# Kernel optimization log

Measured on AMD Instinct MI355X. Metric: run time of the kernel, lower is better.

## Reference

```python
import jax, jax.numpy as jnp
import numpy as np

DIM = 256
H = 4
HD = DIM // H
SCALE = HD ** -0.5
W = 10
PAD = W // 2
MAX_LEN = 512


def setup_inputs() -> dict:
    key = jax.random.key(0)
    ks = jax.random.split(key, 32)
    B, T, D = 32, 512, DIM
    def w(k, shape):
        return jax.random.normal(k, shape, dtype=jnp.float32) * 0.02
    inp = {
        'x': jax.random.normal(ks[0], (B, T, D), dtype=jnp.float32),
        # global TemporalAttention params (weights stored as (in,out))
        'gq_w': w(ks[1], (D, D)), 'gq_b': jnp.zeros((D,), jnp.float32),
        'gk_w': w(ks[2], (D, D)), 'gk_b': jnp.zeros((D,), jnp.float32),
        'gv_w': w(ks[3], (D, D)), 'gv_b': jnp.zeros((D,), jnp.float32),
        'go_w': w(ks[4], (D, D)), 'go_b': jnp.zeros((D,), jnp.float32),
        'rel_pos_bias': w(ks[5], (2 * MAX_LEN - 1, H)),
        # local sliding-window attention params
        'lq_w': w(ks[6], (D, D)), 'lq_b': jnp.zeros((D,), jnp.float32),
        'lk_w': w(ks[7], (D, D)), 'lk_b': jnp.zeros((D,), jnp.float32),
        'lv_w': w(ks[8], (D, D)), 'lv_b': jnp.zeros((D,), jnp.float32),
        # pattern attention (only q/k projections matter for returned weights)
        'pattern_embed': jax.random.normal(ks[9], (1, 3, D), dtype=jnp.float32),
        'pq_w': w(ks[10], (D, D)), 'pq_b': jnp.zeros((D,), jnp.float32),
        'pk_w': w(ks[11], (D, D)), 'pk_b': jnp.zeros((D,), jnp.float32),
        # fusion MLP
        'f1_w': w(ks[12], (2 * D, D)), 'f1_b': jnp.zeros((D,), jnp.float32),
        'f2_w': w(ks[13], (D, D)), 'f2_b': jnp.zeros((D,), jnp.float32),
    }
    return inp


def _forward(x, gq_w, gq_b, gk_w, gk_b, gv_w, gv_b, go_w, go_b, rel_pos_bias,
             lq_w, lq_b, lk_w, lk_b, lv_w, lv_b,
             pattern_embed, pq_w, pq_b, pk_w, pk_b,
             f1_w, f1_b, f2_w, f2_b):
    B, T, D = x.shape
    # ---- global temporal attention ----
    q = (x @ gq_w + gq_b).reshape(B, T, H, HD)
    k = (x @ gk_w + gk_b).reshape(B, T, H, HD)
    v = (x @ gv_w + gv_b).reshape(B, T, H, HD)
    attn = jnp.einsum('bthd,bshd->bhts', q, k) * SCALE  # (B,H,T,T)
    pos = jnp.arange(T)
    idx = jnp.clip(pos[None, :] - pos[:, None] + T - 1, 0, 2 * T - 2)  # (T,T)
    attn = attn + jnp.transpose(rel_pos_bias[idx], (2, 0, 1))[None]
    attn_w = jax.nn.softmax(attn, axis=-1)  # dropout = identity in eval
    g_out = jnp.einsum('bhts,bshd->bthd', attn_w, v).reshape(B, T, D)
    global_out = g_out @ go_w + go_b
    # ---- local sliding-window attention (single head over full dim) ----
    x_pad = jnp.pad(x, ((0, 0), (PAD, PAD), (0, 0)))  # zero pad -> k/v get bias
    lq = x @ lq_w + lq_b                      # (B,T,D)
    lk = x_pad @ lk_w + lk_b                  # (B,T+W,D)
    lv = x_pad @ lv_w + lv_b
    widx = jnp.arange(T)[:, None] + jnp.arange(W)[None, :]  # (T,W)
    k_win = lk[:, widx]                       # (B,T,W,D)
    v_win = lv[:, widx]
    l_attn = jax.nn.softmax(jnp.einsum('btd,btwd->btw', lq, k_win) * SCALE, axis=-1)
    local_out = jnp.einsum('btw,btwd->btd', l_attn, v_win)
    # ---- fusion MLP + residual ----
    fused = jnp.concatenate([global_out, local_out], axis=-1)
    output = jax.nn.relu(fused @ f1_w + f1_b) @ f2_w + f2_b + x
    # ---- pattern attention (torch MHA, weights averaged over heads) ----
    pe = jnp.broadcast_to(pattern_embed, (B, 3, D))
    pooled = jnp.mean(x, axis=1, keepdims=True)  # (B,1,D)
    pq = (pooled @ pq_w + pq_b).reshape(B, 1, H, HD)
    pk = (pe @ pk_w + pk_b).reshape(B, 3, H, HD)
    plogits = jnp.einsum('bqhd,bkhd->bhqk', pq, pk) * SCALE  # (B,H,1,3)
    pw = jax.nn.softmax(plogits, axis=-1).mean(axis=1)  # avg over heads -> (B,1,3)
    pattern_scores = pw[:, 0]  # (B,3)
    return output, pattern_scores


def reference(x, gq_w, gq_b, gk_w, gk_b, gv_w, gv_b, go_w, go_b, rel_pos_bias,
              lq_w, lq_b, lk_w, lk_b, lv_w, lv_b,
              pattern_embed, pq_w, pq_b, pk_w, pk_b,
              f1_w, f1_b, f2_w, f2_b):
    return _forward(x, gq_w, gq_b, gk_w, gk_b, gv_w, gv_b, go_w, go_b, rel_pos_bias,
                    lq_w, lq_b, lk_w, lk_b, lv_w, lv_b,
                    pattern_embed, pq_w, pq_b, pk_w, pk_b,
                    f1_w, f1_b, f2_w, f2_b)
```

## Files before the change

### kernel.cpp

```cpp
#include <hip/hip_runtime.h>
#include <hip/hip_bf16.h>

typedef __attribute__((ext_vector_type(8))) __bf16 bf16x8;
typedef __attribute__((ext_vector_type(8))) unsigned short u16x8;
typedef __attribute__((ext_vector_type(4))) float f32x4;

#define MFMA_BF16(a,b,c) __builtin_amdgcn_mfma_f32_16x16x32_bf16((a),(b),(c),0,0,0)

#define ASCALE 0.125f
#define SEQT 512
#define NB 32
#define BT 16384

#define GLD_LDS16(g, l) __builtin_amdgcn_global_load_lds( \
    (__attribute__((address_space(1))) void*)(g), \
    (__attribute__((address_space(3))) void*)(l), 16, 0, 0)

__device__ __forceinline__ unsigned short f2bf(float f) {
    unsigned int u = __float_as_uint(f);
    u += 0x7fffu + ((u >> 16) & 1u);
    return (unsigned short)(u >> 16);
}
__device__ __forceinline__ float bf2f(unsigned short h) {
    return __uint_as_float(((unsigned int)h) << 16);
}

__global__ __launch_bounds__(256) void cast_x_kernel(const float* __restrict__ x,
                                                     unsigned short* __restrict__ xb, int n) {
    int i = (blockIdx.x * 256 + threadIdx.x) * 4;
    if (i < n) {
        float4 v = *(const float4*)(x + i);
        ushort4 o;
        o.x = f2bf(v.x); o.y = f2bf(v.y); o.z = f2bf(v.z); o.w = f2bf(v.w);
        *(ushort4*)(xb + i) = o;
    }
}

struct WPack {
    const float* src[9];
    unsigned short* dst[9];
    int K[9];
    const float* bsrc[5];
    float* bdst;
};

__global__ __launch_bounds__(256) void wconv_all(WPack p) {
    const int z = blockIdx.z;
    const int tid = threadIdx.x;
    if (z == 9) {
        int idx = blockIdx.y * 8 + blockIdx.x;
        if (idx < 5) p.bdst[idx * 256 + tid] = p.bsrc[idx][tid];
        return;
    }
    const int K = p.K[z];
    const int k0 = blockIdx.x * 64;
    if (k0 >= K) return;
    const int n0 = blockIdx.y * 64;
    __shared__ float tile[64][65];
    const int tx = tid & 63, ty = tid >> 6;
    const float* src = p.src[z];
    #pragma unroll
    for (int i = 0; i < 16; ++i) {
        int r = ty * 16 + i;
        tile[r][tx] = src[(size_t)(k0 + r) * 256 + n0 + tx];
    }
    __syncthreads();
    unsigned short* dst = p.dst[z];
    #pragma unroll
    for (int i = 0; i < 16; ++i) {
        int r = ty * 16 + i;
        dst[(size_t)(n0 + r) * K + k0 + tx] = f2bf(tile[tx][r]);
    }
}

template<int BM, int BN>
__global__ __launch_bounds__(256)
void gemm_v3(const unsigned short* __restrict__ A, const unsigned short* __restrict__ Bt,
             const float* __restrict__ bias, int K,
             void* __restrict__ out, int ldc, int mode, int do_relu, int bias_row,
             const float* __restrict__ resid) {
    constexpr int CA = BM / 32;
    constexpr int CB = BN / 32;
    constexpr int MFM = 4;
    constexpr int MFN = (BM == 128) ? 4 : 2;
    __shared__ __align__(16) unsigned short As[2][BM * 64];
    __shared__ __align__(16) unsigned short Bs[2][BN * 64];
    const int tid = threadIdx.x;
    const int w = tid >> 6, l = tid & 63, g = l >> 4, rl = l & 15;
    const int wrow = (BM == 128) ? (w >> 1) * 64 : 0;
    const int wcol = (BM == 128) ? (w & 1) * 64 : w * 32;
    const int m0 = blockIdx.x * BM, n0 = blockIdx.y * BN;

    f32x4 acc[MFM][MFN];
    #pragma unroll
    for (int m = 0; m < MFM; ++m)
        #pragma unroll
        for (int n = 0; n < MFN; ++n) acc[m][n] = (f32x4){0.f, 0.f, 0.f, 0.f};

    auto stage = [&](int buf, int k0) {
        #pragma unroll
        for (int j = 0; j < CA; ++j) {
            int e = j * 256 + tid;
            int r = e >> 3, sp = e & 7;
            int kc = (sp ^ (r & 7)) * 8;
            GLD_LDS16(A + (size_t)(m0 + r) * K + k0 + kc, &As[buf][e * 8]);
        }
        #pragma unroll
        for (int j = 0; j < CB; ++j) {
            int e = j * 256 + tid;
            int r = e >> 3, sp = e & 7;
            int kc = (sp ^ (r & 7)) * 8;
            GLD_LDS16(Bt + (size_t)(n0 + r) * K + k0 + kc, &Bs[buf][e * 8]);
        }
    };

    const int NIT = K >> 6;
    stage(0, 0);
    const int sx = (rl & 7);
    for (int it = 0; it < NIT; ++it) {
        const int cur = it & 1;
        if (it + 1 < NIT) {
            stage(cur ^ 1, (it + 1) << 6);
            asm volatile("s_waitcnt vmcnt(%0)" :: "n"(CA + CB) : "memory");
        } else {
            asm volatile("s_waitcnt vmcnt(0)" ::: "memory");
        }
        __builtin_amdgcn_s_barrier();
        #pragma unroll
        for (int kk = 0; kk < 2; ++kk) {
            const int co = ((kk * 4 + g) ^ sx) * 8;
            bf16x8 af[MFM], bf_[MFN];
            #pragma unroll
            for (int m = 0; m < MFM; ++m)
                af[m] = *(const bf16x8*)&As[cur][(wrow + m * 16 + rl) * 64 + co];
            #pragma unroll
            for (int n = 0; n < MFN; ++n)
                bf_[n] = *(const bf16x8*)&Bs[cur][(wcol + n * 16 + rl) * 64 + co];
            #pragma unroll
            for (int m = 0; m < MFM; ++m)
                #pragma unroll
                for (int n = 0; n < MFN; ++n)
                    acc[m][n] = MFMA_BF16(af[m], bf_[n], acc[m][n]);
        }
        __builtin_amdgcn_s_barrier();
    }

    #pragma unroll
    for (int m = 0; m < MFM; ++m) {
        #pragma unroll
        for (int n = 0; n < MFN; ++n) {
            #pragma unroll
            for (int r = 0; r < 4; ++r) {
                int row = m0 + wrow + m * 16 + g * 4 + r;
                int col = n0 + wcol + n * 16 + rl;
                float v = acc[m][n][r] + (bias_row ? bias[row] : bias[col]);
                if (do_relu) v = fmaxf(v, 0.f);
                if (mode == 0) {
                    ((unsigned short*)out)[(size_t)row * ldc + col] = f2bf(v);
                } else {
                    float res = resid ? resid[(size_t)row * ldc + col] : 0.f;
                    ((float*)out)[(size_t)row * ldc + col] = v + res;
                }
            }
        }
    }
}

__global__ __launch_bounds__(256)
void attn_global2(const unsigned short* __restrict__ proj, const unsigned short* __restrict__ vT,
                  const float* __restrict__ rpb, unsigned short* __restrict__ gout) {
    __shared__ __align__(16) unsigned short Ks[64][72];
    __shared__ __align__(16) unsigned short Vs[64][72];
    __shared__ __align__(16) unsigned short Ps[64][72];
    __shared__ float rb_s[127];

    const int tid = threadIdx.x;
    const int w = tid >> 6, l = tid & 63, g = l >> 4, rl = l & 15;
    const int bh = blockIdx.y, b = bh >> 2, h = bh & 3;
    const int t0 = blockIdx.x * 64;

    bf16x8 qf[2];
    #pragma unroll
    for (int kk = 0; kk < 2; ++kk)
        qf[kk] = *(const bf16x8*)(proj + (size_t)(b * SEQT + t0 + w * 16 + rl) * 1280
                                  + h * 64 + kk * 32 + g * 8);

    f32x4 oacc[4];
    #pragma unroll
    for (int n = 0; n < 4; ++n) oacc[n] = (f32x4){0.f, 0.f, 0.f, 0.f};
    float lpart[4] = {0.f, 0.f, 0.f, 0.f};

    for (int s0 = 0; s0 < SEQT; s0 += 64) {
        __syncthreads();
        #pragma unroll
        for (int cc = 0; cc < 2; ++cc) {
            int c = tid + cc * 256;
            int sr = c >> 3, hc = c & 7;
            u16x8 kv = *(const u16x8*)(proj + (size_t)(b * SEQT + s0 + sr) * 1280
                                       + 256 + h * 64 + hc * 8);
            *(u16x8*)&Ks[sr][hc * 8] = kv;
            u16x8 vv = *(const u16x8*)(vT + (size_t)(h * 64 + sr) * BT
                                       + b * SEQT + s0 + hc * 8);
            *(u16x8*)&Vs[sr][hc * 8] = vv;
        }
        if (tid < 127) {
            int dd = s0 - t0 + 448 + tid;
            rb_s[tid] = rpb[dd * 4 + h];
        }
        __syncthreads();

        f32x4 sacc[4];
        #pragma unroll
        for (int n = 0; n < 4; ++n) sacc[n] = (f32x4){0.f, 0.f, 0.f, 0.f};
        #pragma unroll
        for (int kk = 0; kk < 2; ++kk) {
            #pragma unroll
            for (int n = 0; n < 4; ++n) {
                bf16x8 kf = *(const bf16x8*)&Ks[n * 16 + rl][kk * 32 + g * 8];
                sacc[n] = MFMA_BF16(qf[kk], kf, sacc[n]);
            }
        }

        #pragma unroll
        for (int n = 0; n < 4; ++n) {
            #pragma unroll
            for (int r = 0; r < 4; ++r) {
                int relc = (n * 16 + rl) - (w * 16 + g * 4 + r) + 63;
                float p = __expf(sacc[n][r] * ASCALE + rb_s[relc]);
                lpart[r] += p;
                Ps[w * 16 + g * 4 + r][n * 16 + rl] = f2bf(p);
            }
        }

        #pragma unroll
        for (int kk = 0; kk < 2; ++kk) {
            bf16x8 pf = *(const bf16x8*)&Ps[w * 16 + rl][kk * 32 + g * 8];
            #pragma unroll
            for (int n = 0; n < 4; ++n) {
                bf16x8 vf = *(const bf16x8*)&Vs[n * 16 + rl][kk * 32 + g * 8];
                oacc[n] = MFMA_BF16(pf, vf, oacc[n]);
            }
        }
    }

    #pragma unroll
    for (int r = 0; r < 4; ++r) {
        #pragma unroll
        for (int mk = 1; mk < 16; mk <<= 1) lpart[r] += __shfl_xor(lpart[r], mk);
    }
    const size_t obase = (size_t)b * SEQT * 256 + h * 64;
    #pragma unroll
    for (int n = 0; n < 4; ++n) {
        #pragma unroll
        for (int r = 0; r < 4; ++r) {
            float o = oacc[n][r] / lpart[r];
            gout[obase + (size_t)(t0 + w * 16 + g * 4 + r) * 256 + n * 16 + rl] = f2bf(o);
        }
    }
}

__global__ __launch_bounds__(256)
void local_attn(const unsigned short* __restrict__ proj,
                const float* __restrict__ lk_bias, const float* __restrict__ lv_bias,
                unsigned short* __restrict__ fused) {
    const int tid = threadIdx.x;
    const int wv = tid >> 6, lane = tid & 63;
    const int row = blockIdx.x * 4 + wv;
    const int b = row >> 9, tt = row & 511;

    ushort4 qv = *((const ushort4*)(proj + (size_t)row * 1280 + 512) + lane);
    float qf[4] = {bf2f(qv.x), bf2f(qv.y), bf2f(qv.z), bf2f(qv.w)};

    float sw[10];
    #pragma unroll
    for (int w = 0; w < 10; ++w) {
        int src = tt + w - 5;
        float kf[4];
        if (src >= 0 && src < 512) {
            ushort4 kv = *((const ushort4*)(proj + (size_t)(b * 512 + src) * 1280 + 768) + lane);
            kf[0] = bf2f(kv.x); kf[1] = bf2f(kv.y); kf[2] = bf2f(kv.z); kf[3] = bf2f(kv.w);
        } else {
            float4 kb4 = *((const float4*)lk_bias + lane);
            kf[0] = kb4.x; kf[1] = kb4.y; kf[2] = kb4.z; kf[3] = kb4.w;
        }
        float p = qf[0] * kf[0] + qf[1] * kf[1] + qf[2] * kf[2] + qf[3] * kf[3];
        #pragma unroll
        for (int mk = 1; mk < 64; mk <<= 1) p += __shfl_xor(p, mk);
        sw[w] = p * ASCALE;
    }
    float mx = sw[0];
    #pragma unroll
    for (int w = 1; w < 10; ++w) mx = fmaxf(mx, sw[w]);
    float pv[10], s = 0.f;
    #pragma unroll
    for (int w = 0; w < 10; ++w) { pv[w] = __expf(sw[w] - mx); s += pv[w]; }
    float inv = 1.f / s;

    float of[4] = {0.f, 0.f, 0.f, 0.f};
    #pragma unroll
    for (int w = 0; w < 10; ++w) {
        int src = tt + w - 5;
        float vf[4];
        if (src >= 0 && src < 512) {
            ushort4 vv = *((const ushort4*)(proj + (size_t)(b * 512 + src) * 1280 + 1024) + lane);
            vf[0] = bf2f(vv.x); vf[1] = bf2f(vv.y); vf[2] = bf2f(vv.z); vf[3] = bf2f(vv.w);
        } else {
            float4 vb4 = *((const float4*)lv_bias + lane);
            vf[0] = vb4.x; vf[1] = vb4.y; vf[2] = vb4.z; vf[3] = vb4.w;
        }
        float pw = pv[w] * inv;
        of[0] += pw * vf[0]; of[1] += pw * vf[1]; of[2] += pw * vf[2]; of[3] += pw * vf[3];
    }
    ushort4 o;
    o.x = f2bf(of[0]); o.y = f2bf(of[1]); o.z = f2bf(of[2]); o.w = f2bf(of[3]);
    *((ushort4*)(fused + (size_t)row * 512 + 256) + lane) = o;
}

__global__ __launch_bounds__(256)
void pooled_part(const unsigned short* __restrict__ xb, float* __restrict__ pp) {
    int b = blockIdx.x >> 3, tc = blockIdx.x & 7;
    int d = threadIdx.x;
    const unsigned short* xp = xb + ((size_t)b * SEQT + tc * 64) * 256 + d;
    float s = 0.f;
    #pragma unroll 8
    for (int t = 0; t < 64; ++t) s += bf2f(xp[(size_t)t * 256]);
    pp[(size_t)(tc * 32 + b) * 256 + d] = s * (1.0f / 512.0f);
}

__global__ __launch_bounds__(256)
void pattern_k(const float* __restrict__ pp, const float* __restrict__ pe,
               const float* __restrict__ pq_w, const float* __restrict__ pq_b,
               const float* __restrict__ pk_w, const float* __restrict__ pk_b,
               float* __restrict__ out_scores) {
    __shared__ float pool_s[256];
    __shared__ float pes[3 * 256];
    __shared__ float pq_s[256];
    __shared__ float pk_s[3][256];
    __shared__ float pw_s[4][3];
    int b = blockIdx.x, d = threadIdx.x;
    float ps = 0.f;
    #pragma unroll
    for (int tc = 0; tc < 8; ++tc) ps += pp[(size_t)(tc * 32 + b) * 256 + d];
    pool_s[d] = ps;
    pes[d] = pe[d]; pes[256 + d] = pe[256 + d]; pes[512 + d] = pe[512 + d];
    __syncthreads();
    float acc = pq_b[d];
    for (int k = 0; k < 256; ++k) acc += pool_s[k] * pq_w[k * 256 + d];
    pq_s[d] = acc;
    for (int j = 0; j < 3; ++j) {
        float a = pk_b[d];
        for (int k = 0; k < 256; ++k) a += pes[j * 256 + k] * pk_w[k * 256 + d];
        pk_s[j][d] = a;
    }
    __syncthreads();
    int h = d >> 6, lane = d & 63;
    float lg[3];
    #pragma unroll
    for (int j = 0; j < 3; ++j) {
        float p = pq_s[h * 64 + lane] * pk_s[j][h * 64 + lane];
        #pragma unroll
        for (int mk = 1; mk < 64; mk <<= 1) p += __shfl_xor(p, mk);
        lg[j] = p * ASCALE;
    }
    float mx = fmaxf(fmaxf(lg[0], lg[1]), lg[2]);
    float e0 = __expf(lg[0] - mx), e1 = __expf(lg[1] - mx), e2 = __expf(lg[2] - mx);
    float sinv = 1.f / (e0 + e1 + e2);
    if (lane == 0) { pw_s[h][0] = e0 * sinv; pw_s[h][1] = e1 * sinv; pw_s[h][2] = e2 * sinv; }
    __syncthreads();
    if (d < 3)
        out_scores[b * 3 + d] = 0.25f * (pw_s[0][d] + pw_s[1][d] + pw_s[2][d] + pw_s[3][d]);
}

extern "C" void kernel_launch(void* const* d_in, const int* in_sizes, int n_in,
                              void* d_out, int out_size, void* d_ws, size_t ws_size,
                              hipStream_t stream) {
    (void)in_sizes; (void)n_in; (void)out_size; (void)ws_size;
    const float* x    = (const float*)d_in[0];
    const float* gq_w = (const float*)d_in[1];  const float* gq_b = (const float*)d_in[2];
    const float* gk_w = (const float*)d_in[3];  const float* gk_b = (const float*)d_in[4];
    const float* gv_w = (const float*)d_in[5];  const float* gv_b = (const float*)d_in[6];
    const float* go_w = (const float*)d_in[7];  const float* go_b = (const float*)d_in[8];
    const float* rpb  = (const float*)d_in[9];
    const float* lq_w = (const float*)d_in[10]; const float* lq_b = (const float*)d_in[11];
    const float* lk_w = (const float*)d_in[12]; const float* lk_b = (const float*)d_in[13];
    const float* lv_w = (const float*)d_in[14]; const float* lv_b = (const float*)d_in[15];
    const float* pe   = (const float*)d_in[16];
    const float* pq_w = (const float*)d_in[17]; const float* pq_b = (const float*)d_in[18];
    const float* pk_w = (const float*)d_in[19]; const float* pk_b = (const float*)d_in[20];
    const float* f1_w = (const float*)d_in[21]; const float* f1_b = (const float*)d_in[22];
    const float* f2_w = (const float*)d_in[23]; const float* f2_b = (const float*)d_in[24];

    char* ws = (char*)d_ws;
    const size_t MB = 1024 * 1024;
    unsigned short* xb    = (unsigned short*)(ws + 0);
    unsigned short* proj  = (unsigned short*)(ws + 8 * MB);
    unsigned short* vT    = (unsigned short*)(ws + 48 * MB);
    unsigned short* fused = (unsigned short*)(ws + 56 * MB);
    unsigned short* hb    = (unsigned short*)(ws + 72 * MB);
    unsigned short* wts   = (unsigned short*)(ws + 80 * MB);
    unsigned short* gv_t  = wts;
    unsigned short* go_t  = gv_t + 65536;
    unsigned short* f1_t  = go_t + 65536;
    unsigned short* f2_t  = f1_t + 131072;
    unsigned short* wcat  = f2_t + 65536;
    float* bcat = (float*)(ws + 82 * MB);
    float* pp   = (float*)(ws + 83 * MB);

    float* out = (float*)d_out;
    float* out_scores = out + (size_t)BT * 256;

    cast_x_kernel<<<4096, 256, 0, stream>>>(x, xb, BT * 256);
    WPack p;
    p.src[0] = gq_w; p.dst[0] = wcat + 0 * 65536; p.K[0] = 256;
    p.src[1] = gk_w; p.dst[1] = wcat + 1 * 65536; p.K[1] = 256;
    p.src[2] = lq_w; p.dst[2] = wcat + 2 * 65536; p.K[2] = 256;
    p.src[3] = lk_w; p.dst[3] = wcat + 3 * 65536; p.K[3] = 256;
    p.src[4] = lv_w; p.dst[4] = wcat + 4 * 65536; p.K[4] = 256;
    p.src[5] = gv_w; p.dst[5] = gv_t;  p.K[5] = 256;
    p.src[6] = go_w; p.dst[6] = go_t;  p.K[6] = 256;
    p.src[7] = f1_w; p.dst[7] = f1_t;  p.K[7] = 512;
    p.src[8] = f2_w; p.dst[8] = f2_t;  p.K[8] = 256;
    p.bsrc[0] = gq_b; p.bsrc[1] = gk_b; p.bsrc[2] = lq_b; p.bsrc[3] = lk_b; p.bsrc[4] = lv_b;
    p.bdst = bcat;
    wconv_all<<<dim3(8, 4, 10), 256, 0, stream>>>(p);
    pooled_part<<<256, 256, 0, stream>>>(xb, pp);

    gemm_v3<128, 128><<<dim3(BT / 128, 10), 256, 0, stream>>>(xb, wcat, bcat, 256, proj, 1280, 0, 0, 0, nullptr);
    gemm_v3<64, 128><<<dim3(4, BT / 128), 256, 0, stream>>>(gv_t, xb, gv_b, 256, vT, BT, 0, 0, 1, nullptr);

    attn_global2<<<dim3(SEQT / 64, NB * 4), 256, 0, stream>>>(proj, vT, rpb, xb);

    gemm_v3<64, 128><<<dim3(BT / 64, 2), 256, 0, stream>>>(xb, go_t, go_b, 256, fused, 512, 0, 0, 0, nullptr);

    local_attn<<<BT / 4, 256, 0, stream>>>(proj, lk_b, lv_b, fused);

    gemm_v3<64, 128><<<dim3(BT / 64, 2), 256, 0, stream>>>(fused, f1_t, f1_b, 512, hb, 256, 0, 1, 0, nullptr);
    gemm_v3<64, 128><<<dim3(BT / 64, 2), 256, 0, stream>>>(hb, f2_t, f2_b, 256, out, 256, 1, 0, 0, x);

    pattern_k<<<NB, 256, 0, stream>>>(pp, pe, pq_w, pq_b, pk_w, pk_b, out_scores);
}
```

Baseline: 306.2 us.

## Fold output projection into first fusion MLP weight and retile GEMM to K=32

Precomputes go_w·f1_w[:256] as a combined weight (and the matching folded bias) so the global-attention output projection GEMM is removed. Attention now writes straight into the fused buffer, and the first MLP GEMM uses the combined weight. The GEMM kernel is also rewritten with a K-step of 32 and a 2x2 wave layout with configurable leading dimensions. The folded weight is rounded to bf16, which adds a little rounding error. The smaller K tile doubles the loop iterations and barriers.

```diff
diff --git a/kernel.cpp b/kernel.cpp
--- a/kernel.cpp
+++ b/kernel.cpp
@@ -42,6 +42,7 @@
     int K[9];
     const float* bsrc[5];
     float* bdst;
+    unsigned short* w1cat;
 };
 
 __global__ __launch_bounds__(256) void wconv_all(WPack p) {
@@ -56,39 +57,59 @@
     const int k0 = blockIdx.x * 64;
     if (k0 >= K) return;
     const int n0 = blockIdx.y * 64;
-    __shared__ float tile[64][65];
     const int tx = tid & 63, ty = tid >> 6;
     const float* src = p.src[z];
+    unsigned short* dst = p.dst[z];
+    if (z == 6) {
+        #pragma unroll
+        for (int i = 0; i < 16; ++i) {
+            int r = ty * 16 + i;
+            dst[(size_t)(k0 + r) * 256 + n0 + tx] = f2bf(src[(size_t)(k0 + r) * 256 + n0 + tx]);
+        }
+        return;
+    }
+    __shared__ float tile[64][65];
     #pragma unroll
     for (int i = 0; i < 16; ++i) {
         int r = ty * 16 + i;
         tile[r][tx] = src[(size_t)(k0 + r) * 256 + n0 + tx];
     }
     __syncthreads();
-    unsigned short* dst = p.dst[z];
     #pragma unroll
     for (int i = 0; i < 16; ++i) {
         int r = ty * 16 + i;
-        dst[(size_t)(n0 + r) * K + k0 + tx] = f2bf(tile[tx][r]);
-    }
-}
-
-template<int BM, int BN>
-__global__ __launch_bounds__(256)
-void gemm_v3(const unsigned short* __restrict__ A, const unsigned short* __restrict__ Bt,
+        unsigned short v = f2bf(tile[tx][r]);
+        dst[(size_t)(n0 + r) * K + k0 + tx] = v;
+        if (z == 7 && k0 >= 256)
+            p.w1cat[(size_t)(n0 + r) * 512 + k0 + tx] = v;
+    }
+}
+
+__global__ __launch_bounds__(256)
+void bias2_k(const float* __restrict__ f1_b, const float* __restrict__ go_b,
+             const float* __restrict__ f1_w, float* __restrict__ f1bp) {
+    int n = threadIdx.x;
+    float s = f1_b[n];
+    for (int k = 0; k < 256; ++k) s += go_b[k] * f1_w[k * 256 + n];
+    f1bp[n] = s;
+}
+
+template<int BM>
+__global__ __launch_bounds__(256)
+void gemm_v5(const unsigned short* __restrict__ A, int lda,
+             const unsigned short* __restrict__ Bt, int ldb,
              const float* __restrict__ bias, int K,
              void* __restrict__ out, int ldc, int mode, int do_relu, int bias_row,
              const float* __restrict__ resid) {
-    constexpr int CA = BM / 32;
-    constexpr int CB = BN / 32;
-    constexpr int MFM = 4;
-    constexpr int MFN = (BM == 128) ? 4 : 2;
-    __shared__ __align__(16) unsigned short As[2][BM * 64];
-    __shared__ __align__(16) unsigned short Bs[2][BN * 64];
+    constexpr int BN = 128;
+    constexpr int AR = BM / 64, BR = BN / 64;
+    constexpr int MFM = BM / 32, MFN = 4;
+    __shared__ __align__(16) unsigned short As[2][BM * 32];
+    __shared__ __align__(16) unsigned short Bs[2][BN * 32];
     const int tid = threadIdx.x;
     const int w = tid >> 6, l = tid & 63, g = l >> 4, rl = l & 15;
-    const int wrow = (BM == 128) ? (w >> 1) * 64 : 0;
-    const int wcol = (BM == 128) ? (w & 1) * 64 : w * 32;
+    const int wrow = (w >> 1) * (BM / 2);
+    const int wcol = (w & 1) * 64;
     const int m0 = blockIdx.x * BM, n0 = blockIdx.y * BN;
 
     f32x4 acc[MFM][MFN];
@@ -99,51 +120,52 @@
 
     auto stage = [&](int buf, int k0) {
         #pragma unroll
-        for (int j = 0; j < CA; ++j) {
+        for (int j = 0; j < AR; ++j) {
             int e = j * 256 + tid;
-            int r = e >> 3, sp = e & 7;
-            int kc = (sp ^ (r & 7)) * 8;
-            GLD_LDS16(A + (size_t)(m0 + r) * K + k0 + kc, &As[buf][e * 8]);
-        }
-        #pragma unroll
-        for (int j = 0; j < CB; ++j) {
+            int r = e >> 2, sp = e & 3;
+            int kc = (sp ^ (r & 3)) * 8;
+            GLD_LDS16(A + (size_t)(m0 + r) * lda + k0 + kc, &As[buf][e * 8]);
+        }
+        #pragma unroll
+        for (int j = 0; j < BR; ++j) {
             int e = j * 256 + tid;
-            int r = e >> 3, sp = e & 7;
-            int kc = (sp ^ (r & 7)) * 8;
-            GLD_LDS16(Bt + (size_t)(n0 + r) * K + k0 + kc, &Bs[buf][e * 8]);
+            int r = e >> 2, sp = e & 3;
+            int kc = (sp ^ (r & 3)) * 8;
+            GLD_LDS16(Bt + (size_t)(n0 + r) * ldb + k0 + kc, &Bs[buf][e * 8]);
         }
     };
 
-    const int NIT = K >> 6;
+    const int NIT = K >> 5;
     stage(0, 0);
-    const int sx = (rl & 7);
+    const int co = ((rl & 3) ^ 0) * 0;
     for (int it = 0; it < NIT; ++it) {
         const int cur = it & 1;
         if (it + 1 < NIT) {
-            stage(cur ^ 1, (it + 1) << 6);
-            asm volatile("s_waitcnt vmcnt(%0)" :: "n"(CA + CB) : "memory");
+            stage(cur ^ 1, (it + 1) << 5);
+            asm volatile("s_waitcnt vmcnt(%0)" :: "n"(AR + BR) : "memory");
         } else {
             asm volatile("s_waitcnt vmcnt(0)" ::: "memory");
         }
         __builtin_amdgcn_s_barrier();
-        #pragma unroll
-        for (int kk = 0; kk < 2; ++kk) {
-            const int co = ((kk * 4 + g) ^ sx) * 8;
-            bf16x8 af[MFM], bf_[MFN];
-            #pragma unroll
-            for (int m = 0; m < MFM; ++m)
-                af[m] = *(const bf16x8*)&As[cur][(wrow + m * 16 + rl) * 64 + co];
+        bf16x8 af[MFM], bf_[MFN];
+        #pragma unroll
+        for (int m = 0; m < MFM; ++m) {
+            int row = wrow + m * 16 + rl;
+            af[m] = *(const bf16x8*)&As[cur][row * 32 + ((g ^ (rl & 3)) * 8)];
+        }
+        #pragma unroll
+        for (int n = 0; n < MFN; ++n) {
+            int row = wcol + n * 16 + rl;
+            bf_[n] = *(const bf16x8*)&Bs[cur][row * 32 + ((g ^ (rl & 3)) * 8)];
+        }
+        #pragma unroll
+        for (int m = 0; m < MFM; ++m)
             #pragma unroll
             for (int n = 0; n < MFN; ++n)
-                bf_[n] = *(const bf16x8*)&Bs[cur][(wcol + n * 16 + rl) * 64 + co];
-            #pragma unroll
-            for (int m = 0; m < MFM; ++m)
-                #pragma unroll
-                for (int n = 0; n < MFN; ++n)
-                    acc[m][n] = MFMA_BF16(af[m], bf_[n], acc[m][n]);
-        }
+                acc[m][n] = MFMA_BF16(af[m], bf_[n], acc[m][n]);
         __builtin_amdgcn_s_barrier();
     }
+    (void)co;
 
     #pragma unroll
     for (int m = 0; m < MFM; ++m) {
@@ -153,7 +175,8 @@
             for (int r = 0; r < 4; ++r) {
                 int row = m0 + wrow + m * 16 + g * 4 + r;
                 int col = n0 + wcol + n * 16 + rl;
-                float v = acc[m][n][r] + (bias_row ? bias[row] : bias[col]);
+                float bv = bias ? (bias_row ? bias[row] : bias[col]) : 0.f;
+                float v = acc[m][n][r] + bv;
                 if (do_relu) v = fmaxf(v, 0.f);
                 if (mode == 0) {
                     ((unsigned short*)out)[(size_t)row * ldc + col] = f2bf(v);
@@ -168,7 +191,7 @@
 
 __global__ __launch_bounds__(256)
 void attn_global2(const unsigned short* __restrict__ proj, const unsigned short* __restrict__ vT,
-                  const float* __restrict__ rpb, unsigned short* __restrict__ gout) {
+                  const float* __restrict__ rpb, unsigned short* __restrict__ gout, int ostride) {
     __shared__ __align__(16) unsigned short Ks[64][72];
     __shared__ __align__(16) unsigned short Vs[64][72];
     __shared__ __align__(16) unsigned short Ps[64][72];
@@ -248,13 +271,13 @@
         #pragma unroll
         for (int mk = 1; mk < 16; mk <<= 1) lpart[r] += __shfl_xor(lpart[r], mk);
     }
-    const size_t obase = (size_t)b * SEQT * 256 + h * 64;
     #pragma unroll
     for (int n = 0; n < 4; ++n) {
         #pragma unroll
         for (int r = 0; r < 4; ++r) {
             float o = oacc[n][r] / lpart[r];
-            gout[obase + (size_t)(t0 + w * 16 + g * 4 + r) * 256 + n * 16 + rl] = f2bf(o);
+            gout[(size_t)(b * SEQT + t0 + w * 16 + g * 4 + r) * ostride
+                 + h * 64 + n * 16 + rl] = f2bf(o);
         }
     }
 }
@@ -399,11 +422,13 @@
     unsigned short* hb    = (unsigned short*)(ws + 72 * MB);
     unsigned short* wts   = (unsigned short*)(ws + 80 * MB);
     unsigned short* gv_t  = wts;
-    unsigned short* go_t  = gv_t + 65536;
-    unsigned short* f1_t  = go_t + 65536;
+    unsigned short* goS   = gv_t + 65536;
+    unsigned short* f1_t  = goS + 65536;
     unsigned short* f2_t  = f1_t + 131072;
     unsigned short* wcat  = f2_t + 65536;
+    unsigned short* w1cat = wcat + 327680;
     float* bcat = (float*)(ws + 82 * MB);
+    float* f1bp = bcat + 2048;
     float* pp   = (float*)(ws + 83 * MB);
 
     float* out = (float*)d_out;
@@ -417,25 +442,32 @@
     p.src[3] = lk_w; p.dst[3] = wcat + 3 * 65536; p.K[3] = 256;
     p.src[4] = lv_w; p.dst[4] = wcat + 4 * 65536; p.K[4] = 256;
     p.src[5] = gv_w; p.dst[5] = gv_t;  p.K[5] = 256;
-    p.src[6] = go_w; p.dst[6] = go_t;  p.K[6] = 256;
+    p.src[6] = go_w; p.dst[6] = goS;   p.K[6] = 256;
     p.src[7] = f1_w; p.dst[7] = f1_t;  p.K[7] = 512;
     p.src[8] = f2_w; p.dst[8] = f2_t;  p.K[8] = 256;
     p.bsrc[0] = gq_b; p.bsrc[1] = gk_b; p.bsrc[2] = lq_b; p.bsrc[3] = lk_b; p.bsrc[4] = lv_b;
     p.bdst = bcat;
+    p.w1cat = w1cat;
     wconv_all<<<dim3(8, 4, 10), 256, 0, stream>>>(p);
+    bias2_k<<<1, 256, 0, stream>>>(f1_b, go_b, f1_w, f1bp);
     pooled_part<<<256, 256, 0, stream>>>(xb, pp);
 
-    gemm_v3<128, 128><<<dim3(BT / 128, 10), 256, 0, stream>>>(xb, wcat, bcat, 256, proj, 1280, 0, 0, 0, nullptr);
-    gemm_v3<64, 128><<<dim3(4, BT / 128), 256, 0, stream>>>(gv_t, xb, gv_b, 256, vT, BT, 0, 0, 1, nullptr);
-
-    attn_global2<<<dim3(SEQT / 64, NB * 4), 256, 0, stream>>>(proj, vT, rpb, xb);
-
-    gemm_v3<64, 128><<<dim3(BT / 64, 2), 256, 0, stream>>>(xb, go_t, go_b, 256, fused, 512, 0, 0, 0, nullptr);
+    gemm_v5<64><<<dim3(4, 2), 256, 0, stream>>>(f1_t, 512, goS, 256, nullptr, 256,
+                                                w1cat, 512, 0, 0, 0, nullptr);
+
+    gemm_v5<128><<<dim3(BT / 128, 10), 256, 0, stream>>>(xb, 256, wcat, 256, bcat, 256,
+                                                         proj, 1280, 0, 0, 0, nullptr);
+    gemm_v5<64><<<dim3(4, BT / 128), 256, 0, stream>>>(gv_t, 256, xb, 256, gv_b, 256,
+                                                       vT, BT, 0, 0, 1, nullptr);
+
+    attn_global2<<<dim3(SEQT / 64, NB * 4), 256, 0, stream>>>(proj, vT, rpb, fused, 512);
 
     local_attn<<<BT / 4, 256, 0, stream>>>(proj, lk_b, lv_b, fused);
 
-    gemm_v3<64, 128><<<dim3(BT / 64, 2), 256, 0, stream>>>(fused, f1_t, f1_b, 512, hb, 256, 0, 1, 0, nullptr);
-    gemm_v3<64, 128><<<dim3(BT / 64, 2), 256, 0, stream>>>(hb, f2_t, f2_b, 256, out, 256, 1, 0, 0, x);
+    gemm_v5<64><<<dim3(BT / 64, 2), 256, 0, stream>>>(fused, 512, w1cat, 512, f1bp, 512,
+                                                      hb, 256, 0, 1, 0, nullptr);
+    gemm_v5<64><<<dim3(BT / 64, 2), 256, 0, stream>>>(hb, 256, f2_t, 256, f2_b, 256,
+                                                      out, 256, 1, 0, 0, x);
 
     pattern_k<<<NB, 256, 0, stream>>>(pp, pe, pq_w, pq_b, pk_w, pk_b, out_scores);
 }
```

Result: no change. 311.7 us (+1.8%).
